# Kernel optimization log

Hardware: AMD Instinct MI355X
Metric: run time of the kernel (lower is better)

## Reference

```python
import jax, jax.numpy as jnp
import numpy as np

N = 10000      # num nodes
R = 16         # num relations
NB = 30        # num bases (hardcoded in source: num_bases=30)
E = 160000     # num edges
IN, HID, OUT = 256, 256, 128


def rgcn_conv(x, src, dst, etype, basis, comp, root, bias):
    """PyG RGCNConv with basis decomposition, aggr='mean' (per relation), root weight + bias."""
    # relation weights from basis decomposition: W_r = sum_b comp[r,b] * basis[b]
    W = jnp.einsum('rb,bio->rio', comp, basis)            # [R, in, out]
    xw = jnp.einsum('ni,rio->rno', x, W)                  # [R, N, out]
    msg = xw[etype, src]                                  # [E, out] gather per edge
    # per-(dst, relation) mean aggregation, then sum over relations
    seg = dst * R + etype                                 # combined segment key
    cnt = jax.ops.segment_sum(jnp.ones((msg.shape[0],), msg.dtype), seg, num_segments=N * R)
    msg = msg / jnp.maximum(cnt[seg], 1.0)[:, None]       # zero-degree -> 0 (matches scatter-mean)
    agg = jax.ops.segment_sum(msg, dst, num_segments=N)   # [N, out]
    return agg + x @ root + bias


def setup_inputs() -> dict:
    key = jax.random.key(0)
    ks = jax.random.split(key, 11)
    g = lambda k, shape, s: jax.random.normal(k, shape, jnp.float32) * s
    s1 = (2.0 / (IN + HID)) ** 0.5
    s2 = (2.0 / (HID + OUT)) ** 0.5
    return dict(
        x=g(ks[0], (N, IN), 1.0),
        edge_index=jax.random.randint(ks[1], (2, E), 0, N),
        edge_type=jax.random.randint(ks[2], (E,), 0, R),
        basis1=g(ks[3], (NB, IN, HID), s1),
        comp1=g(ks[4], (R, NB), 1.0 / NB ** 0.5),
        root1=g(ks[5], (IN, HID), s1),
        bias1=jnp.zeros((HID,), jnp.float32),
        basis2=g(ks[6], (NB, HID, OUT), s2),
        comp2=g(ks[7], (R, NB), 1.0 / NB ** 0.5),
        root2=g(ks[8], (HID, OUT), s2),
        bias2=jnp.zeros((OUT,), jnp.float32),
    )


def reference(x, edge_index, edge_type, basis1, comp1, root1, bias1,
              basis2, comp2, root2, bias2):
    src, dst = edge_index[0], edge_index[1]
    h = jax.nn.relu(rgcn_conv(x, src, dst, edge_type, basis1, comp1, root1, bias1))
    return rgcn_conv(h, src, dst, edge_type, basis2, comp2, root2, bias2)
```

## Files before the change

kernel.cpp:

```cpp
#include <hip/hip_runtime.h>
#include <hip/hip_bf16.h>

#define NN 10000
#define MP 10112
#define RR 16
#define NBASE 30
#define EE 160000
#define HIDF 256
#define OUTF 128
#define NSEG (NN * RR)

typedef __attribute__((ext_vector_type(8))) short bf16x8;
typedef __attribute__((ext_vector_type(4))) short s16x4;
typedef __attribute__((ext_vector_type(4))) float f32x4;

static __device__ __forceinline__ short f2bf(float f) {
    union { float f; unsigned u; } v; v.f = f;
    unsigned r = v.u + 0x7FFFu + ((v.u >> 16) & 1u);
    return (short)(r >> 16);
}
static __device__ __forceinline__ float bf2f(short s) {
    union { unsigned u; float f; } v;
    v.u = ((unsigned)(unsigned short)s) << 16;
    return v.f;
}
static __device__ __forceinline__ void gl16(const short* g, short* l) {
    __builtin_amdgcn_global_load_lds((const __attribute__((address_space(1))) void*)g,
                                     (__attribute__((address_space(3))) void*)l, 16, 0, 0);
}

template <int OUT>
__global__ void wtr_k(const float* __restrict__ basis, const float* __restrict__ comp,
                      const float* __restrict__ root, short* __restrict__ WT) {
    __shared__ short t[32][34];
    const int i0 = blockIdx.x * 32, n0 = blockIdx.y * 32;
    const int r = n0 / OUT, o0 = n0 % OUT;
    const int tx = threadIdx.x & 31, ty = threadIdx.x >> 5;
    #pragma unroll
    for (int dy = 0; dy < 32; dy += 8) {
        const int i = i0 + ty + dy, o = o0 + tx;
        float v;
        if (r < RR) {
            float s = 0.f;
            #pragma unroll
            for (int b = 0; b < NBASE; b++)
                s += comp[r * NBASE + b] * basis[((long)b * 256 + i) * OUT + o];
            v = s;
        } else {
            v = root[(long)i * OUT + o];
        }
        t[ty + dy][tx] = f2bf(v);
    }
    __syncthreads();
    #pragma unroll
    for (int dy = 0; dy < 32; dy += 8)
        WT[(long)(n0 + ty + dy) * 256 + i0 + tx] = t[tx][ty + dy];
}

__global__ void count_k(const int* __restrict__ dst, const int* __restrict__ et,
                        int* __restrict__ cnt) {
    int e = blockIdx.x * 256 + threadIdx.x;
    if (e < EE) atomicAdd(&cnt[dst[e] * RR + et[e]], 1);
}

__global__ void inv_k(const int* __restrict__ cnt, float* __restrict__ invc) {
    int i = blockIdx.x * 256 + threadIdx.x;
    if (i < NSEG) invc[i] = 1.f / (float)max(cnt[i], 1);
}

__global__ void scan1_k(const int* __restrict__ cnt, int* __restrict__ incl,
                        int* __restrict__ bsum) {
    __shared__ int s[256];
    int i = blockIdx.x * 256 + threadIdx.x;
    int v = (i < NSEG) ? cnt[i] : 0;
    s[threadIdx.x] = v;
    __syncthreads();
    for (int off = 1; off < 256; off <<= 1) {
        int u = (threadIdx.x >= off) ? s[threadIdx.x - off] : 0;
        __syncthreads();
        s[threadIdx.x] += u;
        __syncthreads();
    }
    if (i < NSEG) incl[i] = s[threadIdx.x];
    if (threadIdx.x == 255) bsum[blockIdx.x] = s[255];
}

__global__ void scan2_k(int* __restrict__ bsum, int nb) {
    __shared__ int s[1024];
    int t = threadIdx.x;
    s[t] = (t < nb) ? bsum[t] : 0;
    __syncthreads();
    for (int off = 1; off < 1024; off <<= 1) {
        int u = (t >= off) ? s[t - off] : 0;
        __syncthreads();
        s[t] += u;
        __syncthreads();
    }
    if (t < nb) bsum[t] = s[t];
}

__global__ void scan3_k(const int* __restrict__ cnt, const int* __restrict__ incl,
                        const int* __restrict__ bsum, int* __restrict__ row_ptr,
                        int* __restrict__ fillpos) {
    int i = blockIdx.x * 256 + threadIdx.x;
    if (i >= NSEG) return;
    int off = (blockIdx.x > 0) ? bsum[blockIdx.x - 1] : 0;
    int ex = off + incl[i] - cnt[i];
    row_ptr[i] = ex;
    fillpos[i] = ex;
    if (i == 0) row_ptr[NSEG] = EE;
}

__global__ void fill_k(const int* __restrict__ src, const int* __restrict__ dst,
                       const int* __restrict__ et, int* __restrict__ fillpos,
                       const float* __restrict__ invc,
                       int* __restrict__ eoff1, int* __restrict__ eoff2,
                       float* __restrict__ wgt) {
    int e = blockIdx.x * 256 + threadIdx.x;
    if (e < EE) {
        int s = src[e], t = et[e];
        int seg = dst[e] * RR + t;
        int p = atomicAdd(&fillpos[seg], 1);
        eoff1[p] = s * (17 * HIDF) + t * HIDF;
        eoff2[p] = s * (17 * OUTF) + t * OUTF;
        wgt[p] = invc[seg];
    }
}

__global__ void cvtbf_k(const float* __restrict__ X, short* __restrict__ Y) {
    int i = blockIdx.x * 256 + threadIdx.x;
    if (i >= NN * 64) return;
    float4 v = *(const float4*)(X + (long)i * 4);
    s16x4 pk = { f2bf(v.x), f2bf(v.y), f2bf(v.z), f2bf(v.w) };
    *(s16x4*)&Y[(long)i * 4] = pk;
}

template <int NTOT>
__global__ __launch_bounds__(256, 4) void gemm_xw_k(const short* __restrict__ A,
                                                    const short* __restrict__ WT,
                                                    short* __restrict__ XW) {
    constexpr int NBN = NTOT / 128;
    __shared__ __align__(16) short smem[128 * 132];
    short* As = smem;
    short* Bs = smem + 8192;

    const int nwg = gridDim.x;
    const int q = nwg >> 3, r = nwg & 7;
    const int orig = blockIdx.x;
    const int xcd = orig & 7, wi = orig >> 3;
    const int wgid = (xcd < r ? xcd * (q + 1) : r * (q + 1) + (xcd - r) * q) + wi;
    const int m0 = (wgid / NBN) * 128;
    const int n0 = (wgid % NBN) * 128;

    const int tid = threadIdx.x;
    const int lane = tid & 63;
    const int w = tid >> 6;
    const int wr = w >> 1, wc = w & 1;
    const int al = lane & 15;
    const int cl = lane >> 4;

    int gsrc[4];
    #pragma unroll
    for (int i = 0; i < 4; i++) {
        int ci = i * 256 + tid;
        int row = ci >> 3;
        gsrc[i] = row * 256 + (((ci & 7) ^ (row & 7)) << 3);
    }

    int aoff[4][2], boff[4][2];
    #pragma unroll
    for (int f = 0; f < 4; f++)
        #pragma unroll
        for (int k2 = 0; k2 < 2; k2++) {
            int ra = wr * 64 + f * 16 + al;
            aoff[f][k2] = (ra << 6) + ((((k2 << 2) | cl) ^ (ra & 7)) << 3);
            int rb = wc * 64 + f * 16 + al;
            boff[f][k2] = (rb << 6) + ((((k2 << 2) | cl) ^ (rb & 7)) << 3);
        }

    f32x4 acc[4][4] = {};
    const short* abase = A + (long)m0 * 256;
    const short* bbase = WT + (long)n0 * 256;

    #pragma unroll
    for (int kk = 0; kk < 256; kk += 64) {
        #pragma unroll
        for (int i = 0; i < 4; i++)
            gl16(abase + kk + gsrc[i], &As[i * 2048 + w * 512]);
        #pragma unroll
        for (int i = 0; i < 4; i++)
            gl16(bbase + kk + gsrc[i], &Bs[i * 2048 + w * 512]);
        __syncthreads();

        bf16x8 a[4][2], b[4][2];
        #pragma unroll
        for (int f = 0; f < 4; f++)
            #pragma unroll
            for (int k2 = 0; k2 < 2; k2++) {
                a[f][k2] = *(const bf16x8*)&As[aoff[f][k2]];
                b[f][k2] = *(const bf16x8*)&Bs[boff[f][k2]];
            }
        #pragma unroll
        for (int k2 = 0; k2 < 2; k2++)
            #pragma unroll
            for (int fm = 0; fm < 4; fm++)
                #pragma unroll
                for (int fn = 0; fn < 4; fn++)
                    acc[fm][fn] = __builtin_amdgcn_mfma_f32_16x16x32_bf16(
                        a[fm][k2], b[fn][k2], acc[fm][fn], 0, 0, 0);
        __syncthreads();
    }

    #pragma unroll
    for (int fm = 0; fm < 4; fm++) {
        const int rowb = wr * 64 + fm * 16 + (cl << 2);
        #pragma unroll
        for (int fn = 0; fn < 4; fn++) {
            const int col = wc * 64 + fn * 16 + al;
            #pragma unroll
            for (int j = 0; j < 4; j++)
                smem[(rowb + j) * 132 + col] = f2bf(acc[fm][fn][j]);
        }
    }
    __syncthreads();

    #pragma unroll
    for (int pass = 0; pass < 8; pass++) {
        int c = pass * 256 + tid;
        int row = c >> 4, qq = c & 15;
        uint4 v = *(const uint4*)&smem[row * 132 + qq * 8];
        *(uint4*)&XW[(long)(m0 + row) * NTOT + n0 + qq * 8] = v;
    }
}

template <int OUT, bool L1>
__global__ void aggh_k(const int* __restrict__ rowp, const int* __restrict__ eoff,
                       const float* __restrict__ wgt, const short* __restrict__ XW,
                       const float* __restrict__ bias, short* __restrict__ Hout,
                       float* __restrict__ Fout) {
    constexpr int NTOT = 17 * OUT;
    const int n = (blockIdx.x * 256 + threadIdx.x) >> 6;
    const int lane = threadIdx.x & 63;
    if (n >= NN) return;
    const int b = rowp[n * 16], e = rowp[n * 16 + 16];

    if (L1) {
        float a0 = 0.f, a1 = 0.f, a2 = 0.f, a3 = 0.f;
        int j = b;
        for (; j + 1 < e; j += 2) {
            int o0 = eoff[j], o1 = eoff[j + 1];
            float w0 = wgt[j], w1 = wgt[j + 1];
            s16x4 v0 = *(const s16x4*)&XW[(long)o0 + lane * 4];
            s16x4 v1 = *(const s16x4*)&XW[(long)o1 + lane * 4];
            a0 += w0 * bf2f(v0.x) + w1 * bf2f(v1.x);
            a1 += w0 * bf2f(v0.y) + w1 * bf2f(v1.y);
            a2 += w0 * bf2f(v0.z) + w1 * bf2f(v1.z);
            a3 += w0 * bf2f(v0.w) + w1 * bf2f(v1.w);
        }
        if (j < e) {
            int o0 = eoff[j]; float w0 = wgt[j];
            s16x4 v0 = *(const s16x4*)&XW[(long)o0 + lane * 4];
            a0 += w0 * bf2f(v0.x); a1 += w0 * bf2f(v0.y);
            a2 += w0 * bf2f(v0.z); a3 += w0 * bf2f(v0.w);
        }
        s16x4 rt = *(const s16x4*)&XW[(long)n * NTOT + 16 * OUT + lane * 4];
        f32x4 bb = *(const f32x4*)&bias[lane * 4];
        a0 = fmaxf(a0 + bf2f(rt.x) + bb.x, 0.f);
        a1 = fmaxf(a1 + bf2f(rt.y) + bb.y, 0.f);
        a2 = fmaxf(a2 + bf2f(rt.z) + bb.z, 0.f);
        a3 = fmaxf(a3 + bf2f(rt.w) + bb.w, 0.f);
        s16x4 pk = { f2bf(a0), f2bf(a1), f2bf(a2), f2bf(a3) };
        *(s16x4*)&Hout[(long)n * OUT + lane * 4] = pk;
    } else {
        float a0 = 0.f, a1 = 0.f;
        int j = b;
        for (; j + 1 < e; j += 2) {
            int o0 = eoff[j], o1 = eoff[j + 1];
            float w0 = wgt[j], w1 = wgt[j + 1];
            unsigned v0 = *(const unsigned*)&XW[(long)o0 + lane * 2];
            unsigned v1 = *(const unsigned*)&XW[(long)o1 + lane * 2];
            a0 += w0 * bf2f((short)(v0 & 0xffff)) + w1 * bf2f((short)(v1 & 0xffff));
            a1 += w0 * bf2f((short)(v0 >> 16)) + w1 * bf2f((short)(v1 >> 16));
        }
        if (j < e) {
            int o0 = eoff[j]; float w0 = wgt[j];
            unsigned v0 = *(const unsigned*)&XW[(long)o0 + lane * 2];
            a0 += w0 * bf2f((short)(v0 & 0xffff));
            a1 += w0 * bf2f((short)(v0 >> 16));
        }
        unsigned rt = *(const unsigned*)&XW[(long)n * NTOT + 16 * OUT + lane * 2];
        a0 += bf2f((short)(rt & 0xffff)) + bias[lane * 2];
        a1 += bf2f((short)(rt >> 16)) + bias[lane * 2 + 1];
        float2 st = { a0, a1 };
        *(float2*)&Fout[(long)n * OUT + lane * 2] = st;
    }
}

extern "C" void kernel_launch(void* const* d_in, const int* in_sizes, int n_in,
                              void* d_out, int out_size, void* d_ws, size_t ws_size,
                              hipStream_t stream) {
    const float* x      = (const float*)d_in[0];
    const int*   ei     = (const int*)d_in[1];
    const int*   et     = (const int*)d_in[2];
    const float* basis1 = (const float*)d_in[3];
    const float* comp1  = (const float*)d_in[4];
    const float* root1  = (const float*)d_in[5];
    const float* bias1  = (const float*)d_in[6];
    const float* basis2 = (const float*)d_in[7];
    const float* comp2  = (const float*)d_in[8];
    const float* root2  = (const float*)d_in[9];
    const float* bias2  = (const float*)d_in[10];
    const int* src = ei;
    const int* dst = ei + EE;

    char* p = (char*)d_ws;
    auto take = [&](size_t bytes) { char* q = p; p += (bytes + 255) & ~(size_t)255; return q; };
    short* XW    = (short*)take((size_t)MP * 17 * HIDF * 2);
    short* WT1   = (short*)take((size_t)17 * HIDF * 256 * 2);
    short* WT2   = (short*)take((size_t)17 * OUTF * 256 * 2);
    short* Xbf   = (short*)take((size_t)MP * 256 * 2);
    short* Hbf   = (short*)take((size_t)MP * 256 * 2);
    int*   cnt   = (int*)take((size_t)NSEG * 4);
    float* invc  = (float*)take((size_t)NSEG * 4);
    int*   incl  = (int*)take((size_t)NSEG * 4);
    int*   rowp  = (int*)take((size_t)(NSEG + 1) * 4);
    int*   fpos  = (int*)take((size_t)NSEG * 4);
    int*   bsum  = (int*)take(1024 * 4);
    int*   eoff1 = (int*)take((size_t)EE * 4);
    int*   eoff2 = (int*)take((size_t)EE * 4);
    float* wgt   = (float*)take((size_t)EE * 4);

    const int NB1 = (NSEG + 255) / 256;

    hipMemsetAsync(cnt, 0, (size_t)NSEG * 4, stream);

    {
        dim3 g1(256 / 32, 17 * HIDF / 32), g2(256 / 32, 17 * OUTF / 32);
        wtr_k<HIDF><<<g1, 256, 0, stream>>>(basis1, comp1, root1, WT1);
        wtr_k<OUTF><<<g2, 256, 0, stream>>>(basis2, comp2, root2, WT2);
    }

    count_k<<<(EE + 255) / 256, 256, 0, stream>>>(dst, et, cnt);
    inv_k<<<NB1, 256, 0, stream>>>(cnt, invc);
    scan1_k<<<NB1, 256, 0, stream>>>(cnt, incl, bsum);
    scan2_k<<<1, 1024, 0, stream>>>(bsum, NB1);
    scan3_k<<<NB1, 256, 0, stream>>>(cnt, incl, bsum, rowp, fpos);
    fill_k<<<(EE + 255) / 256, 256, 0, stream>>>(src, dst, et, fpos, invc, eoff1, eoff2, wgt);

    cvtbf_k<<<(NN * 64 + 255) / 256, 256, 0, stream>>>(x, Xbf);

    gemm_xw_k<17 * HIDF><<<(MP / 128) * (17 * HIDF / 128), 256, 0, stream>>>(Xbf, WT1, XW);
    aggh_k<HIDF, true><<<(NN * 64) / 256, 256, 0, stream>>>(rowp, eoff1, wgt, XW, bias1, Hbf, nullptr);

    gemm_xw_k<17 * OUTF><<<(MP / 128) * (17 * OUTF / 128), 256, 0, stream>>>(Hbf, WT2, XW);
    aggh_k<OUTF, false><<<(NN * 64) / 256, 256, 0, stream>>>(rowp, eoff2, wgt, XW, bias2, nullptr, (float*)d_out);
}
```

Measured before the change: 146.5 us.

## Shrink GEMM tiles to 64x64, fold inverse-count into scan, unroll gather by four

The XW GEMM tile drops from 128x128 to 64x64 with 2x2 MFMA fragments per wave, half the shared memory and launch bounds raised to 8 blocks per CU, giving many more workgroups. The separate inverse-count kernel is merged into scan3, removing one launch. The aggregation loops now issue four independent gathers per iteration instead of two, to keep more loads in flight. Smaller tiles cut register and LDS pressure but reload A and B more often and lower reuse per block.

Measured after the change: 141.4 us. -3.5%, faster.

```diff
diff --git a/kernel.cpp b/kernel.cpp
--- a/kernel.cpp
+++ b/kernel.cpp
@@ -63,11 +63,6 @@
     if (e < EE) atomicAdd(&cnt[dst[e] * RR + et[e]], 1);
 }
 
-__global__ void inv_k(const int* __restrict__ cnt, float* __restrict__ invc) {
-    int i = blockIdx.x * 256 + threadIdx.x;
-    if (i < NSEG) invc[i] = 1.f / (float)max(cnt[i], 1);
-}
-
 __global__ void scan1_k(const int* __restrict__ cnt, int* __restrict__ incl,
                         int* __restrict__ bsum) {
     __shared__ int s[256];
@@ -101,13 +96,15 @@
 
 __global__ void scan3_k(const int* __restrict__ cnt, const int* __restrict__ incl,
                         const int* __restrict__ bsum, int* __restrict__ row_ptr,
-                        int* __restrict__ fillpos) {
+                        int* __restrict__ fillpos, float* __restrict__ invc) {
     int i = blockIdx.x * 256 + threadIdx.x;
     if (i >= NSEG) return;
+    int c = cnt[i];
     int off = (blockIdx.x > 0) ? bsum[blockIdx.x - 1] : 0;
-    int ex = off + incl[i] - cnt[i];
+    int ex = off + incl[i] - c;
     row_ptr[i] = ex;
     fillpos[i] = ex;
+    invc[i] = 1.f / (float)max(c, 1);
     if (i == 0) row_ptr[NSEG] = EE;
 }
 
@@ -136,21 +133,19 @@
 }
 
 template <int NTOT>
-__global__ __launch_bounds__(256, 4) void gemm_xw_k(const short* __restrict__ A,
+__global__ __launch_bounds__(256, 8) void gemm_xw_k(const short* __restrict__ A,
                                                     const short* __restrict__ WT,
                                                     short* __restrict__ XW) {
-    constexpr int NBN = NTOT / 128;
-    __shared__ __align__(16) short smem[128 * 132];
-    short* As = smem;
-    short* Bs = smem + 8192;
+    constexpr int NBN = NTOT / 64;
+    __shared__ __align__(16) short smem[8192];
 
     const int nwg = gridDim.x;
     const int q = nwg >> 3, r = nwg & 7;
     const int orig = blockIdx.x;
     const int xcd = orig & 7, wi = orig >> 3;
     const int wgid = (xcd < r ? xcd * (q + 1) : r * (q + 1) + (xcd - r) * q) + wi;
-    const int m0 = (wgid / NBN) * 128;
-    const int n0 = (wgid % NBN) * 128;
+    const int m0 = (wgid / NBN) * 64;
+    const int n0 = (wgid % NBN) * 64;
 
     const int tid = threadIdx.x;
     const int lane = tid & 63;
@@ -159,76 +154,75 @@
     const int al = lane & 15;
     const int cl = lane >> 4;
 
-    int gsrc[4];
-    #pragma unroll
-    for (int i = 0; i < 4; i++) {
+    int gsrc[2];
+    #pragma unroll
+    for (int i = 0; i < 2; i++) {
         int ci = i * 256 + tid;
         int row = ci >> 3;
         gsrc[i] = row * 256 + (((ci & 7) ^ (row & 7)) << 3);
     }
 
-    int aoff[4][2], boff[4][2];
-    #pragma unroll
-    for (int f = 0; f < 4; f++)
+    int aoff[2][2], boff[2][2];
+    #pragma unroll
+    for (int f = 0; f < 2; f++)
         #pragma unroll
         for (int k2 = 0; k2 < 2; k2++) {
-            int ra = wr * 64 + f * 16 + al;
+            int ra = wr * 32 + f * 16 + al;
             aoff[f][k2] = (ra << 6) + ((((k2 << 2) | cl) ^ (ra & 7)) << 3);
-            int rb = wc * 64 + f * 16 + al;
+            int rb = wc * 32 + f * 16 + al;
             boff[f][k2] = (rb << 6) + ((((k2 << 2) | cl) ^ (rb & 7)) << 3);
         }
 
-    f32x4 acc[4][4] = {};
+    f32x4 acc[2][2] = {};
     const short* abase = A + (long)m0 * 256;
     const short* bbase = WT + (long)n0 * 256;
 
     #pragma unroll
     for (int kk = 0; kk < 256; kk += 64) {
         #pragma unroll
-        for (int i = 0; i < 4; i++)
-            gl16(abase + kk + gsrc[i], &As[i * 2048 + w * 512]);
-        #pragma unroll
-        for (int i = 0; i < 4; i++)
-            gl16(bbase + kk + gsrc[i], &Bs[i * 2048 + w * 512]);
-        __syncthreads();
-
-        bf16x8 a[4][2], b[4][2];
-        #pragma unroll
-        for (int f = 0; f < 4; f++)
+        for (int i = 0; i < 2; i++) {
+            gl16(abase + kk + gsrc[i], &smem[i * 2048 + w * 512]);
+            gl16(bbase + kk + gsrc[i], &smem[4096 + i * 2048 + w * 512]);
+        }
+        __syncthreads();
+
+        bf16x8 a[2][2], b[2][2];
+        #pragma unroll
+        for (int f = 0; f < 2; f++)
             #pragma unroll
             for (int k2 = 0; k2 < 2; k2++) {
-                a[f][k2] = *(const bf16x8*)&As[aoff[f][k2]];
-                b[f][k2] = *(const bf16x8*)&Bs[boff[f][k2]];
+                a[f][k2] = *(const bf16x8*)&smem[aoff[f][k2]];
+                b[f][k2] = *(const bf16x8*)&smem[4096 + boff[f][k2]];
             }
         #pragma unroll
         for (int k2 = 0; k2 < 2; k2++)
             #pragma unroll
-            for (int fm = 0; fm < 4; fm++)
+            for (int fm = 0; fm < 2; fm++)
                 #pragma unroll
-                for (int fn = 0; fn < 4; fn++)
+                for (int fn = 0; fn < 2; fn++)
                     acc[fm][fn] = __builtin_amdgcn_mfma_f32_16x16x32_bf16(
                         a[fm][k2], b[fn][k2], acc[fm][fn], 0, 0, 0);
         __syncthreads();
     }
 
     #pragma unroll
-    for (int fm = 0; fm < 4; fm++) {
-        const int rowb = wr * 64 + fm * 16 + (cl << 2);
-        #pragma unroll
-        for (int fn = 0; fn < 4; fn++) {
-            const int col = wc * 64 + fn * 16 + al;
+    for (int fm = 0; fm < 2; fm++) {
+        const int rowb = wr * 32 + fm * 16 + (cl << 2);
+        #pragma unroll
+        for (int fn = 0; fn < 2; fn++) {
+            const int col = wc * 32 + fn * 16 + al;
             #pragma unroll
             for (int j = 0; j < 4; j++)
-                smem[(rowb + j) * 132 + col] = f2bf(acc[fm][fn][j]);
+                smem[(rowb + j) * 68 + col] = f2bf(acc[fm][fn][j]);
         }
     }
     __syncthreads();
 
     #pragma unroll
-    for (int pass = 0; pass < 8; pass++) {
+    for (int pass = 0; pass < 2; pass++) {
         int c = pass * 256 + tid;
-        int row = c >> 4, qq = c & 15;
-        uint4 v = *(const uint4*)&smem[row * 132 + qq * 8];
+        int row = c >> 3, qq = c & 7;
+        uint4 v = *(const uint4*)&smem[row * 68 + qq * 8];
         *(uint4*)&XW[(long)(m0 + row) * NTOT + n0 + qq * 8] = v;
     }
 }
@@ -247,17 +241,18 @@
     if (L1) {
         float a0 = 0.f, a1 = 0.f, a2 = 0.f, a3 = 0.f;
         int j = b;
-        for (; j + 1 < e; j += 2) {
-            int o0 = eoff[j], o1 = eoff[j + 1];
-            float w0 = wgt[j], w1 = wgt[j + 1];
-            s16x4 v0 = *(const s16x4*)&XW[(long)o0 + lane * 4];
-            s16x4 v1 = *(const s16x4*)&XW[(long)o1 + lane * 4];
-            a0 += w0 * bf2f(v0.x) + w1 * bf2f(v1.x);
-            a1 += w0 * bf2f(v0.y) + w1 * bf2f(v1.y);
-            a2 += w0 * bf2f(v0.z) + w1 * bf2f(v1.z);
-            a3 += w0 * bf2f(v0.w) + w1 * bf2f(v1.w);
-        }
-        if (j < e) {
+        for (; j + 3 < e; j += 4) {
+            s16x4 v0 = *(const s16x4*)&XW[(long)eoff[j] + lane * 4];
+            s16x4 v1 = *(const s16x4*)&XW[(long)eoff[j + 1] + lane * 4];
+            s16x4 v2 = *(const s16x4*)&XW[(long)eoff[j + 2] + lane * 4];
+            s16x4 v3 = *(const s16x4*)&XW[(long)eoff[j + 3] + lane * 4];
+            float w0 = wgt[j], w1 = wgt[j + 1], w2 = wgt[j + 2], w3 = wgt[j + 3];
+            a0 += w0 * bf2f(v0.x) + w1 * bf2f(v1.x) + w2 * bf2f(v2.x) + w3 * bf2f(v3.x);
+            a1 += w0 * bf2f(v0.y) + w1 * bf2f(v1.y) + w2 * bf2f(v2.y) + w3 * bf2f(v3.y);
+            a2 += w0 * bf2f(v0.z) + w1 * bf2f(v1.z) + w2 * bf2f(v2.z) + w3 * bf2f(v3.z);
+            a3 += w0 * bf2f(v0.w) + w1 * bf2f(v1.w) + w2 * bf2f(v2.w) + w3 * bf2f(v3.w);
+        }
+        for (; j < e; j++) {
             int o0 = eoff[j]; float w0 = wgt[j];
             s16x4 v0 = *(const s16x4*)&XW[(long)o0 + lane * 4];
             a0 += w0 * bf2f(v0.x); a1 += w0 * bf2f(v0.y);
@@ -274,15 +269,18 @@
     } else {
         float a0 = 0.f, a1 = 0.f;
         int j = b;
-        for (; j + 1 < e; j += 2) {
-            int o0 = eoff[j], o1 = eoff[j + 1];
-            float w0 = wgt[j], w1 = wgt[j + 1];
-            unsigned v0 = *(const unsigned*)&XW[(long)o0 + lane * 2];
-            unsigned v1 = *(const unsigned*)&XW[(long)o1 + lane * 2];
-            a0 += w0 * bf2f((short)(v0 & 0xffff)) + w1 * bf2f((short)(v1 & 0xffff));
-            a1 += w0 * bf2f((short)(v0 >> 16)) + w1 * bf2f((short)(v1 >> 16));
-        }
-        if (j < e) {
+        for (; j + 3 < e; j += 4) {
+            unsigned v0 = *(const unsigned*)&XW[(long)eoff[j] + lane * 2];
+            unsigned v1 = *(const unsigned*)&XW[(long)eoff[j + 1] + lane * 2];
+            unsigned v2 = *(const unsigned*)&XW[(long)eoff[j + 2] + lane * 2];
+            unsigned v3 = *(const unsigned*)&XW[(long)eoff[j + 3] + lane * 2];
+            float w0 = wgt[j], w1 = wgt[j + 1], w2 = wgt[j + 2], w3 = wgt[j + 3];
+            a0 += w0 * bf2f((short)(v0 & 0xffff)) + w1 * bf2f((short)(v1 & 0xffff))
+                + w2 * bf2f((short)(v2 & 0xffff)) + w3 * bf2f((short)(v3 & 0xffff));
+            a1 += w0 * bf2f((short)(v0 >> 16)) + w1 * bf2f((short)(v1 >> 16))
+                + w2 * bf2f((short)(v2 >> 16)) + w3 * bf2f((short)(v3 >> 16));
+        }
+        for (; j < e; j++) {
             int o0 = eoff[j]; float w0 = wgt[j];
             unsigned v0 = *(const unsigned*)&XW[(long)o0 + lane * 2];
             a0 += w0 * bf2f((short)(v0 & 0xffff));
@@ -341,17 +339,16 @@
     }
 
     count_k<<<(EE + 255) / 256, 256, 0, stream>>>(dst, et, cnt);
-    inv_k<<<NB1, 256, 0, stream>>>(cnt, invc);
     scan1_k<<<NB1, 256, 0, stream>>>(cnt, incl, bsum);
     scan2_k<<<1, 1024, 0, stream>>>(bsum, NB1);
-    scan3_k<<<NB1, 256, 0, stream>>>(cnt, incl, bsum, rowp, fpos);
+    scan3_k<<<NB1, 256, 0, stream>>>(cnt, incl, bsum, rowp, fpos, invc);
     fill_k<<<(EE + 255) / 256, 256, 0, stream>>>(src, dst, et, fpos, invc, eoff1, eoff2, wgt);
 
     cvtbf_k<<<(NN * 64 + 255) / 256, 256, 0, stream>>>(x, Xbf);
 
-    gemm_xw_k<17 * HIDF><<<(MP / 128) * (17 * HIDF / 128), 256, 0, stream>>>(Xbf, WT1, XW);
+    gemm_xw_k<17 * HIDF><<<(MP / 64) * (17 * HIDF / 64), 256, 0, stream>>>(Xbf, WT1, XW);
     aggh_k<HIDF, true><<<(NN * 64) / 256, 256, 0, stream>>>(rowp, eoff1, wgt, XW, bias1, Hbf, nullptr);
 
-    gemm_xw_k<17 * OUTF><<<(MP / 128) * (17 * OUTF / 128), 256, 0, stream>>>(Hbf, WT2, XW);
+    gemm_xw_k<17 * OUTF><<<(MP / 64) * (17 * OUTF / 64), 256, 0, stream>>>(Hbf, WT2, XW);
     aggh_k<OUTF, false><<<(NN * 64) / 256, 256, 0, stream>>>(rowp, eoff2, wgt, XW, bias2, nullptr, (float*)d_out);
 }
```
